# Kernel tuning notes

Measured on AMD Instinct MI355X. Metric: run time of the kernel, lower is better.

The kernel has to match this reference:

```python
import jax, jax.numpy as jnp
import numpy as np

MAX_POS = 1024  # max_position_embeddings


def setup_inputs() -> dict:
    key = jax.random.key(0)
    k1, k2, k3 = jax.random.split(key, 3)
    B, H, S, D = 2, 16, 1024, 64
    E = H * D  # embed_size = 1024
    query = jax.random.normal(k1, (B, H, S, D), dtype=jnp.float32)
    position_embeddings = jax.random.normal(k2, (2 * MAX_POS - 1, E), dtype=jnp.float32)
    dense_kernel = jax.random.normal(k3, (E, E), dtype=jnp.float32) * 0.02
    return {"query": query, "position_embeddings": position_embeddings, "dense_kernel": dense_kernel}


def _gather_pos_embedding(position_embeddings, seq_length):
    # indices max_pos - S .. max_pos + S - 2, clamped to [0, 2*max_pos - 2]
    idx = jnp.arange(MAX_POS - seq_length, MAX_POS + seq_length - 1)
    max_id = 2 * MAX_POS - 2
    idx = jnp.clip(idx, 0, max_id)  # same effect as the sign-mask clamping in the TF code
    return position_embeddings[idx]  # [2S-1, E]


def reference(query, position_embeddings, dense_kernel):
    B, H, S, D = query.shape
    emb = _gather_pos_embedding(position_embeddings, S)          # [2S-1, E]
    emb = emb @ dense_kernel                                      # Dense, no bias: [2S-1, E]
    emb = emb.reshape(-1, H, D).transpose(1, 0, 2)                # [H, 2S-1, D]
    q = query.reshape(H, -1, D)                                   # faithful raw reshape: [H, B*S, D]
    score = jnp.einsum('hnd,hmd->hnm', q, emb)                    # [H, B*S, 2S-1]
    # Transformer-XL style relative shift via computed flat indices
    rel = jnp.arange(S - 1, 2 * S - 1)[None, :] - jnp.arange(S)[:, None]
    rel = rel + jnp.arange(S)[:, None] * (2 * S - 1)              # [S, S] flat indices into S*(2S-1)
    rel = rel.reshape(-1)
    score = score.reshape(H, B, -1)                               # [H, B, S*(2S-1)]
    score = jnp.take(score, rel, axis=2)                          # [H, B, S*S]
    return score.reshape(B, H, S, S)                              # faithful raw reshape
```

## Files before the change

kernel.cpp:

```cpp
#include <hip/hip_runtime.h>

typedef __bf16 bf16;
typedef __bf16 bf16x4 __attribute__((ext_vector_type(4)));
typedef __bf16 bf16x8 __attribute__((ext_vector_type(8)));
typedef float f32x4 __attribute__((ext_vector_type(4)));

#define SEQ 1024
#define EMB 1024
#define NH 16
#define HD 64
#define M2 2047
#define MPAD 2048

__global__ __launch_bounds__(256) void gemm1_kernel(const float* __restrict__ posEmb,
                                                    const float* __restrict__ W,
                                                    bf16* __restrict__ P) {
  __shared__ bf16 As[64][72];
  __shared__ bf16 Bs[64][72];
  const int tid  = threadIdx.x;
  const int lane = tid & 63;
  const int wave = tid >> 6;
  const int wr = wave >> 1, wc = wave & 1;
  const int m0 = blockIdx.y * 64;
  const int n0 = blockIdx.x * 64;

  f32x4 acc[2][2] = {};

  for (int k0 = 0; k0 < EMB; k0 += 64) {
    {
      const int row = tid >> 2;
      const int c0  = (tid & 3) * 16;
      int g = m0 + row;
      if (g > M2 - 1) g = M2 - 1;
      const float4* src = reinterpret_cast<const float4*>(posEmb + (size_t)g * EMB + k0 + c0);
      #pragma unroll
      for (int i = 0; i < 4; ++i) {
        float4 v = src[i];
        bf16x4 bb = { (bf16)v.x, (bf16)v.y, (bf16)v.z, (bf16)v.w };
        *reinterpret_cast<bf16x4*>(&As[row][c0 + 4 * i]) = bb;
      }
    }
    {
      const int n  = tid & 63;
      const int kg = tid >> 6;
      #pragma unroll
      for (int u = 0; u < 4; ++u) {
        bf16x4 bb;
        #pragma unroll
        for (int e = 0; e < 4; ++e) {
          int k = kg * 16 + u * 4 + e;
          bb[e] = (bf16)W[(size_t)(k0 + k) * EMB + n0 + n];
        }
        *reinterpret_cast<bf16x4*>(&Bs[n][kg * 16 + u * 4]) = bb;
      }
    }
    __syncthreads();
    #pragma unroll
    for (int ks = 0; ks < 2; ++ks) {
      bf16x8 a[2], b[2];
      #pragma unroll
      for (int x = 0; x < 2; ++x) {
        a[x] = *reinterpret_cast<const bf16x8*>(&As[wr * 32 + x * 16 + (lane & 15)][ks * 32 + 8 * (lane >> 4)]);
        b[x] = *reinterpret_cast<const bf16x8*>(&Bs[wc * 32 + x * 16 + (lane & 15)][ks * 32 + 8 * (lane >> 4)]);
      }
      #pragma unroll
      for (int x = 0; x < 2; ++x)
        #pragma unroll
        for (int y = 0; y < 2; ++y)
          acc[x][y] = __builtin_amdgcn_mfma_f32_16x16x32_bf16(a[x], b[y], acc[x][y], 0, 0, 0);
    }
    __syncthreads();
  }

  #pragma unroll
  for (int x = 0; x < 2; ++x)
    #pragma unroll
    for (int y = 0; y < 2; ++y)
      #pragma unroll
      for (int r = 0; r < 4; ++r) {
        int row = m0 + wr * 32 + x * 16 + (lane >> 4) * 4 + r;
        int col = n0 + wc * 32 + y * 16 + (lane & 15);
        P[(size_t)row * EMB + col] = (bf16)acc[x][y][r];
      }
}

__global__ __launch_bounds__(256) void band_kernel(const float* __restrict__ q,
                                                   const bf16* __restrict__ P,
                                                   float* __restrict__ out) {
  __shared__ bf16 Qs[64][72];
  __shared__ bf16 Ps[64][72];
  const int tid  = threadIdx.x;
  const int lane = tid & 63;
  const int wave = tid >> 6;
  const int wr = wave >> 1, wc = wave & 1;

  const int tm = blockIdx.x;
  const int i0 = blockIdx.y * 64;
  const int hb = blockIdx.z;
  const int h  = hb >> 1;
  const int b  = hb & 1;
  const int m0 = (SEQ - 1) - (i0 + 63) + tm * 64;

  {
    const int row = tid >> 2;
    const int c0  = (tid & 3) * 16;
    const float4* src = reinterpret_cast<const float4*>(
        q + ((size_t)(h * (2 * SEQ) + b * SEQ + i0 + row)) * HD + c0);
    #pragma unroll
    for (int i = 0; i < 4; ++i) {
      float4 v = src[i];
      bf16x4 bb = { (bf16)v.x, (bf16)v.y, (bf16)v.z, (bf16)v.w };
      *reinterpret_cast<bf16x4*>(&Qs[row][c0 + 4 * i]) = bb;
    }
  }
  {
    const int row = tid >> 2;
    const int c0  = (tid & 3) * 16;
    const int4* src = reinterpret_cast<const int4*>(P + (size_t)(m0 + row) * EMB + h * HD + c0);
    *reinterpret_cast<int4*>(&Ps[row][c0])     = src[0];
    *reinterpret_cast<int4*>(&Ps[row][c0 + 8]) = src[1];
  }
  __syncthreads();

  f32x4 acc[2][2] = {};
  #pragma unroll
  for (int ks = 0; ks < 2; ++ks) {
    bf16x8 a[2], bb[2];
    #pragma unroll
    for (int x = 0; x < 2; ++x) {
      a[x]  = *reinterpret_cast<const bf16x8*>(&Qs[wr * 32 + x * 16 + (lane & 15)][ks * 32 + 8 * (lane >> 4)]);
      bb[x] = *reinterpret_cast<const bf16x8*>(&Ps[wc * 32 + x * 16 + (lane & 15)][ks * 32 + 8 * (lane >> 4)]);
    }
    #pragma unroll
    for (int x = 0; x < 2; ++x)
      #pragma unroll
      for (int y = 0; y < 2; ++y)
        acc[x][y] = __builtin_amdgcn_mfma_f32_16x16x32_bf16(a[x], bb[y], acc[x][y], 0, 0, 0);
  }

  const size_t outbase = (size_t)hb << 20;
  #pragma unroll
  for (int x = 0; x < 2; ++x)
    #pragma unroll
    for (int y = 0; y < 2; ++y)
      #pragma unroll
      for (int r = 0; r < 4; ++r) {
        int il = wr * 32 + x * 16 + (lane >> 4) * 4 + r;
        int ml = wc * 32 + y * 16 + (lane & 15);
        int i = i0 + il;
        int m = m0 + ml;
        int j = m - (SEQ - 1) + i;
        if (j >= 0 && j < SEQ)
          out[outbase + (size_t)i * SEQ + j] = acc[x][y][r];
      }
}

extern "C" void kernel_launch(void* const* d_in, const int* in_sizes, int n_in,
                              void* d_out, int out_size, void* d_ws, size_t ws_size,
                              hipStream_t stream) {
  const float* query  = (const float*)d_in[0];
  const float* posEmb = (const float*)d_in[1];
  const float* W      = (const float*)d_in[2];
  float* out = (float*)d_out;
  bf16* P = (bf16*)d_ws;

  gemm1_kernel<<<dim3(16, 32), 256, 0, stream>>>(posEmb, W, P);
  band_kernel<<<dim3(17, 16, 32), 256, 0, stream>>>(query, P, out);
}
```

Baseline: 63.92 us.

## Loop band kernel over m-tiles with double-buffered async LDS loads and registered Q

The band kernel now processes 8-9 consecutive m-tiles per block instead of one tile per block. Q fragments are loaded once straight into registers. P tiles are streamed into a double-buffered, XOR-swizzled LDS buffer using global_load_lds, so the next tile's load overlaps the current tile's MFMA work and stores. This is meant to cut per-block launch and Q reload overhead and hide P load latency. The cost is fewer blocks (1024 instead of 8704), which lowers parallelism, plus a per-iteration barrier.

```diff
diff --git a/kernel.cpp b/kernel.cpp
--- a/kernel.cpp
+++ b/kernel.cpp
@@ -10,7 +10,6 @@
 #define NH 16
 #define HD 64
 #define M2 2047
-#define MPAD 2048
 
 __global__ __launch_bounds__(256) void gemm1_kernel(const float* __restrict__ posEmb,
                                                     const float* __restrict__ W,
@@ -84,75 +83,104 @@
       }
 }
 
-__global__ __launch_bounds__(256) void band_kernel(const float* __restrict__ q,
-                                                   const bf16* __restrict__ P,
-                                                   float* __restrict__ out) {
-  __shared__ bf16 Qs[64][72];
-  __shared__ bf16 Ps[64][72];
+__global__ __launch_bounds__(256) void band2_kernel(const float* __restrict__ q,
+                                                    const bf16* __restrict__ P,
+                                                    float* __restrict__ out) {
+  __shared__ bf16 Pbuf[2][64 * 64];
   const int tid  = threadIdx.x;
   const int lane = tid & 63;
   const int wave = tid >> 6;
   const int wr = wave >> 1, wc = wave & 1;
 
-  const int tm = blockIdx.x;
-  const int i0 = blockIdx.y * 64;
-  const int hb = blockIdx.z;
+  const int i0 = blockIdx.x * 64;
+  const int hb = blockIdx.y;
   const int h  = hb >> 1;
   const int b  = hb & 1;
-  const int m0 = (SEQ - 1) - (i0 + 63) + tm * 64;
 
+  bf16x8 a[2][2];
   {
-    const int row = tid >> 2;
-    const int c0  = (tid & 3) * 16;
-    const float4* src = reinterpret_cast<const float4*>(
-        q + ((size_t)(h * (2 * SEQ) + b * SEQ + i0 + row)) * HD + c0);
+    const float* qbase = q + ((size_t)(h * (2 * SEQ) + b * SEQ)) * HD;
+    const int row = i0 + wr * 32 + (lane & 15);
+    const int kof = 8 * (lane >> 4);
     #pragma unroll
-    for (int i = 0; i < 4; ++i) {
-      float4 v = src[i];
-      bf16x4 bb = { (bf16)v.x, (bf16)v.y, (bf16)v.z, (bf16)v.w };
-      *reinterpret_cast<bf16x4*>(&Qs[row][c0 + 4 * i]) = bb;
+    for (int x = 0; x < 2; ++x)
+      #pragma unroll
+      for (int ks = 0; ks < 2; ++ks) {
+        const float* src = qbase + (size_t)(row + x * 16) * HD + ks * 32 + kof;
+        float4 v0 = *reinterpret_cast<const float4*>(src);
+        float4 v1 = *reinterpret_cast<const float4*>(src + 4);
+        bf16x8 f = { (bf16)v0.x, (bf16)v0.y, (bf16)v0.z, (bf16)v0.w,
+                     (bf16)v1.x, (bf16)v1.y, (bf16)v1.z, (bf16)v1.w };
+        a[x][ks] = f;
+      }
+  }
+
+  const int m_base = (SEQ - 1) - (i0 + 63);
+  const int tb = blockIdx.z * 9;
+  const int te = (blockIdx.z == 0) ? 9 : 17;
+
+  auto STAGE = [&](int bi, int t) {
+    const int m0 = m_base + t * 64;
+    const char* Pb = reinterpret_cast<const char*>(P);
+    #pragma unroll
+    for (int i = 0; i < 2; ++i) {
+      int s   = wave * 128 + i * 64 + lane;
+      int row = s >> 3;
+      int cs  = s & 7;
+      int cd  = cs ^ (row & 7);
+      const void* g = Pb + ((size_t)(m0 + row) * EMB + h * HD) * 2 + cd * 16;
+      char* l = reinterpret_cast<char*>(&Pbuf[bi][0]) + (wave * 128 + i * 64) * 16;
+      __builtin_amdgcn_global_load_lds(
+          (const __attribute__((address_space(1))) void*)g,
+          (__attribute__((address_space(3))) void*)l, 16, 0, 0);
     }
-  }
-  {
-    const int row = tid >> 2;
-    const int c0  = (tid & 3) * 16;
-    const int4* src = reinterpret_cast<const int4*>(P + (size_t)(m0 + row) * EMB + h * HD + c0);
-    *reinterpret_cast<int4*>(&Ps[row][c0])     = src[0];
-    *reinterpret_cast<int4*>(&Ps[row][c0 + 8]) = src[1];
-  }
+  };
+
+  const size_t outbase = (size_t)hb << 20;
+
+  STAGE(0, tb);
   __syncthreads();
 
-  f32x4 acc[2][2] = {};
-  #pragma unroll
-  for (int ks = 0; ks < 2; ++ks) {
-    bf16x8 a[2], bb[2];
+  int cur = 0;
+  for (int t = tb; t < te; ++t) {
+    if (t + 1 < te) STAGE(cur ^ 1, t + 1);
+
+    const char* buf = reinterpret_cast<const char*>(&Pbuf[cur][0]);
+    f32x4 acc[2][2] = {};
     #pragma unroll
-    for (int x = 0; x < 2; ++x) {
-      a[x]  = *reinterpret_cast<const bf16x8*>(&Qs[wr * 32 + x * 16 + (lane & 15)][ks * 32 + 8 * (lane >> 4)]);
-      bb[x] = *reinterpret_cast<const bf16x8*>(&Ps[wc * 32 + x * 16 + (lane & 15)][ks * 32 + 8 * (lane >> 4)]);
+    for (int ks = 0; ks < 2; ++ks) {
+      bf16x8 bb[2];
+      #pragma unroll
+      for (int y = 0; y < 2; ++y) {
+        int mrow  = wc * 32 + y * 16 + (lane & 15);
+        int chunk = ks * 4 + (lane >> 4);
+        int sw    = chunk ^ (mrow & 7);
+        bb[y] = *reinterpret_cast<const bf16x8*>(buf + mrow * 128 + sw * 16);
+      }
+      #pragma unroll
+      for (int x = 0; x < 2; ++x)
+        #pragma unroll
+        for (int y = 0; y < 2; ++y)
+          acc[x][y] = __builtin_amdgcn_mfma_f32_16x16x32_bf16(a[x][ks], bb[y], acc[x][y], 0, 0, 0);
     }
+
+    const int m0 = m_base + t * 64;
     #pragma unroll
     for (int x = 0; x < 2; ++x)
       #pragma unroll
       for (int y = 0; y < 2; ++y)
-        acc[x][y] = __builtin_amdgcn_mfma_f32_16x16x32_bf16(a[x], bb[y], acc[x][y], 0, 0, 0);
+        #pragma unroll
+        for (int r = 0; r < 4; ++r) {
+          int i = i0 + wr * 32 + x * 16 + (lane >> 4) * 4 + r;
+          int m = m0 + wc * 32 + y * 16 + (lane & 15);
+          int j = m - (SEQ - 1) + i;
+          if ((unsigned)j < SEQ)
+            out[outbase + (size_t)i * SEQ + j] = acc[x][y][r];
+        }
+
+    __syncthreads();
+    cur ^= 1;
   }
-
-  const size_t outbase = (size_t)hb << 20;
-  #pragma unroll
-  for (int x = 0; x < 2; ++x)
-    #pragma unroll
-    for (int y = 0; y < 2; ++y)
-      #pragma unroll
-      for (int r = 0; r < 4; ++r) {
-        int il = wr * 32 + x * 16 + (lane >> 4) * 4 + r;
-        int ml = wc * 32 + y * 16 + (lane & 15);
-        int i = i0 + il;
-        int m = m0 + ml;
-        int j = m - (SEQ - 1) + i;
-        if (j >= 0 && j < SEQ)
-          out[outbase + (size_t)i * SEQ + j] = acc[x][y][r];
-      }
 }
 
 extern "C" void kernel_launch(void* const* d_in, const int* in_sizes, int n_in,
@@ -165,5 +193,5 @@
   bf16* P = (bf16*)d_ws;
 
   gemm1_kernel<<<dim3(16, 32), 256, 0, stream>>>(posEmb, W, P);
-  band_kernel<<<dim3(17, 16, 32), 256, 0, stream>>>(query, P, out);
+  band2_kernel<<<dim3(16, 32, 2), 256, 0, stream>>>(query, P, out);
 }
```

After: 61.26 us. 4.2% less time.
